# Performance work log

Measured on AMD Instinct MI355X. Metric: run time of the kernel, lower is better.

The kernel has to match this reference:

```python
import jax, jax.numpy as jnp
import numpy as np

DIM = 1024
NUM_HEADS = 16
HEAD_DIM = DIM // NUM_HEADS
SCALE = HEAD_DIM ** -0.5


def setup_inputs() -> dict:
    key = jax.random.key(0)
    ks = jax.random.split(key, 9)
    s = DIM ** -0.5
    return {
        'x_q': jax.random.normal(ks[0], (4, 2048, DIM), dtype=jnp.float32),
        'wq': jax.random.normal(ks[1], (DIM, DIM), dtype=jnp.float32) * s,
        'bq': jax.random.normal(ks[2], (DIM,), dtype=jnp.float32) * 0.02,
        'wk': jax.random.normal(ks[3], (DIM, DIM), dtype=jnp.float32) * s,
        'bk': jax.random.normal(ks[4], (DIM,), dtype=jnp.float32) * 0.02,
        'wv': jax.random.normal(ks[5], (DIM, DIM), dtype=jnp.float32) * s,
        'bv': jax.random.normal(ks[6], (DIM,), dtype=jnp.float32) * 0.02,
        'wo': jax.random.normal(ks[7], (DIM, DIM), dtype=jnp.float32) * s,
        'bo': jax.random.normal(ks[8], (DIM,), dtype=jnp.float32) * 0.02,
    }


def reference(x_q, wq, bq, wk, bk, wv, bv, wo, bo):
    B, N, C = x_q.shape
    H, c = NUM_HEADS, HEAD_DIM
    # torch nn.Linear: y = x @ W.T + b, W is [out, in]
    q = (x_q @ wq.T + bq).reshape(B, N, H, c).transpose(0, 2, 1, 3)  # [B,H,N,c]
    k = (x_q @ wk.T + bk).reshape(B, N, H, c).transpose(0, 2, 1, 3)
    v = (x_q @ wv.T + bv).reshape(B, N, H, c).transpose(0, 2, 1, 3)
    attn = jnp.einsum('bhqc,bhkc->bhqk', q, k) * SCALE  # [B,H,N,N]
    attn = jax.nn.softmax(attn, axis=-1)
    out = jnp.einsum('bhqk,bhkc->bhqc', attn, v)  # [B,H,N,c]
    out = out.transpose(0, 2, 1, 3).reshape(B, N, C)
    return out @ wo.T + bo
```

## Files before the change

### kernel.cpp

```cpp
#include <hip/hip_runtime.h>
#include <hip/hip_bf16.h>

typedef __bf16 bf16x8 __attribute__((ext_vector_type(8)));
typedef __bf16 bf16x4 __attribute__((ext_vector_type(4)));
typedef short short4v __attribute__((ext_vector_type(4)));
typedef float f32x4 __attribute__((ext_vector_type(4)));

#define QSCALE 0.18033688011112042f

__device__ __forceinline__ void gload16(const void* g, void* l) {
  __builtin_amdgcn_global_load_lds(
      (const __attribute__((address_space(1))) uint32_t*)g,
      (__attribute__((address_space(3))) uint32_t*)l, 16, 0, 0);
}

__device__ __forceinline__ unsigned bf16bits(float f) {
  union { __bf16 h; unsigned short u; } c; c.h = (__bf16)f; return c.u;
}

__device__ __forceinline__ float exp2_raw(float x) {
  float r;
  asm("v_exp_f32 %0, %1" : "=v"(r) : "v"(x));
  return r;
}

__device__ __forceinline__ f32x4 mfma16(bf16x4 a, bf16x4 b, f32x4 c) {
#if __has_builtin(__builtin_amdgcn_mfma_f32_16x16x16bf16_1k)
  union { bf16x4 h; short4v s; } ua, ub;
  ua.h = a; ub.h = b;
  return __builtin_amdgcn_mfma_f32_16x16x16bf16_1k(ua.s, ub.s, c, 0, 0, 0);
#else
  asm("v_mfma_f32_16x16x16_bf16 %0, %1, %2, %0" : "+v"(c) : "v"(a), "v"(b));
  return c;
#endif
}

__global__ __launch_bounds__(256) void cast_all(
    const float* __restrict__ x, const float* __restrict__ wq, const float* __restrict__ wk,
    const float* __restrict__ wv, const float* __restrict__ wo,
    __bf16* __restrict__ xbf, __bf16* __restrict__ wqb, __bf16* __restrict__ wkb,
    __bf16* __restrict__ wvb, __bf16* __restrict__ wob) {
  int b = blockIdx.x;
  const float* src;
  __bf16* dst;
  int i;
  if (b < 4096) {
    src = x; dst = xbf; i = b * 256 + threadIdx.x;
  } else {
    int s = (b - 4096) >> 9;
    i = ((b - 4096) & 511) * 256 + threadIdx.x;
    src = (s == 0) ? wq : (s == 1) ? wk : (s == 2) ? wv : wo;
    dst = (s == 0) ? wqb : (s == 1) ? wkb : (s == 2) ? wvb : wob;
  }
  const float4* p = (const float4*)src;
  float4 a = p[2 * i], c = p[2 * i + 1];
  bf16x8 v;
  v[0] = (__bf16)a.x; v[1] = (__bf16)a.y; v[2] = (__bf16)a.z; v[3] = (__bf16)a.w;
  v[4] = (__bf16)c.x; v[5] = (__bf16)c.y; v[6] = (__bf16)c.z; v[7] = (__bf16)c.w;
  ((bf16x8*)dst)[i] = v;
}

template <int MODE>
__global__ __launch_bounds__(256) void gemm_nt(
    const __bf16* __restrict__ A,
    const __bf16* __restrict__ W0, const __bf16* __restrict__ W1, const __bf16* __restrict__ W2,
    const float* __restrict__ b0, const float* __restrict__ b1, const float* __restrict__ b2,
    __bf16* __restrict__ o0, __bf16* __restrict__ o1, __bf16* __restrict__ o2,
    float* __restrict__ of) {
  __shared__ __bf16 lA[128 * 32];
  __shared__ __bf16 lB[128 * 32];
  const int t = threadIdx.x;
  const int lane = t & 63;
  const int w = t >> 6;
  const int wr = w >> 1, wc = w & 1;
  const int l16 = lane & 15, l4 = lane >> 4;
  const int m0 = blockIdx.x * 128;
  int sel, bn;
  if (MODE == 0) { sel = blockIdx.y >> 3; bn = (blockIdx.y & 7) * 128; }
  else           { sel = 0;               bn = blockIdx.y * 128; }
  const __bf16* W   = (sel == 0) ? W0 : (sel == 1) ? W1 : W2;
  const float* bias = (sel == 0) ? b0 : (sel == 1) ? b1 : b2;

  f32x4 acc[4][4] = {};

  for (int k0 = 0; k0 < 1024; k0 += 32) {
    __syncthreads();
#pragma unroll
    for (int i = 0; i < 2; i++) {
      int c = t + i * 256;
      int r = c >> 2, cp = c & 3;
      gload16(A + (size_t)(m0 + r) * 1024 + k0 + cp * 8, lA + c * 8);
      gload16(W + (size_t)(bn + r) * 1024 + k0 + cp * 8, lB + c * 8);
    }
    __syncthreads();
    bf16x8 af[4], bfr[4];
#pragma unroll
    for (int m = 0; m < 4; m++)
      af[m] = *(const bf16x8*)(lA + (wr * 64 + m * 16 + l16) * 32 + l4 * 8);
#pragma unroll
    for (int n = 0; n < 4; n++)
      bfr[n] = *(const bf16x8*)(lB + (wc * 64 + n * 16 + l16) * 32 + l4 * 8);
#pragma unroll
    for (int m = 0; m < 4; m++)
#pragma unroll
      for (int n = 0; n < 4; n++)
        acc[m][n] = __builtin_amdgcn_mfma_f32_16x16x32_bf16(af[m], bfr[n], acc[m][n], 0, 0, 0);
  }

  const float scl = (MODE == 0 && sel == 0) ? QSCALE : 1.0f;
  __bf16* outp = (sel == 0) ? o0 : (sel == 1) ? o1 : o2;
#pragma unroll
  for (int n = 0; n < 4; n++) {
    const int col = bn + wc * 64 + n * 16 + l16;
    const float bv = bias[col];
    if (MODE == 0 && sel == 2) {
      const int h = col >> 6, hc = col & 63;
#pragma unroll
      for (int m = 0; m < 4; m++) {
        const int nnb = m0 + wr * 64 + m * 16 + l4 * 4;
        const int b_ = nnb >> 11, nn = nnb & 2047;
        ushort4 ov;
        ov.x = (unsigned short)bf16bits(acc[m][n][0] + bv);
        ov.y = (unsigned short)bf16bits(acc[m][n][1] + bv);
        ov.z = (unsigned short)bf16bits(acc[m][n][2] + bv);
        ov.w = (unsigned short)bf16bits(acc[m][n][3] + bv);
        *(ushort4*)(outp + ((size_t)(b_ * 16 + h) * 64 + hc) * 2048 + nn) = ov;
      }
    } else {
#pragma unroll
      for (int m = 0; m < 4; m++) {
#pragma unroll
        for (int j = 0; j < 4; j++) {
          const int row = m0 + wr * 64 + m * 16 + l4 * 4 + j;
          float v = acc[m][n][j] + bv;
          if (MODE == 0) {
            v *= scl;
            int b_ = row >> 11, nn = row & 2047;
            int h = col >> 6, hc = col & 63;
            outp[(((size_t)(b_ * 16 + h)) * 2048 + nn) * 64 + hc] = (__bf16)v;
          } else {
            of[(size_t)row * 1024 + col] = v;
          }
        }
      }
    }
  }
}

__global__ __launch_bounds__(256) void attn_fwd(const __bf16* __restrict__ Q,
                                                const __bf16* __restrict__ K,
                                                const __bf16* __restrict__ Vt,
                                                __bf16* __restrict__ O) {
  __shared__ __bf16 sm[16384];
  const int flat = blockIdx.x;
  const int wg = (flat & 7) * 128 + (flat >> 3);
  const int bh = wg >> 4;
  const int q0 = (wg & 15) * 128;
  const __bf16* Qh = Q + (size_t)bh * 2048 * 64;
  const __bf16* Kh = K + (size_t)bh * 2048 * 64;
  const __bf16* Vh = Vt + (size_t)bh * 64 * 2048;
  const int t = threadIdx.x, lane = t & 63, w = t >> 6;
  const int l16 = lane & 15, l4 = lane >> 4;

  bf16x8 qf[2][2];
#pragma unroll
  for (int st = 0; st < 2; st++)
#pragma unroll
    for (int kk = 0; kk < 2; kk++)
      qf[st][kk] = *(const bf16x8*)(Qh + (size_t)(q0 + w * 32 + st * 16 + l16) * 64 + kk * 32 + l4 * 8);

  f32x4 ao[2][4] = {};
  float rs[2] = {0.f, 0.f};

  const int rdbase = l4 * 512 + l16 * 8;
  const int vbase = 8192 + (l4 >> 1) * 512 + l16 * 8 + (l4 & 1) * 4;

#pragma unroll
  for (int i = 0; i < 2; i++) {
    int ic = w * 2 + i;
    gload16(Kh + (size_t)lane * 64 + ic * 8, sm + ic * 512 + lane * 8);
    gload16(Vh + (size_t)lane * 2048 + ic * 8, sm + 8192 + ic * 512 + lane * 8);
  }
  __syncthreads();

#define ATTN_STEP(CUR, TNEXT)                                                         \
  {                                                                                   \
    const __bf16* lds = sm + (CUR) * 4096;                                            \
    if ((TNEXT) < 32) {                                                               \
      const int kvn = (TNEXT) * 64;                                                   \
      __bf16* dst = sm + ((CUR) ^ 1) * 4096;                                          \
      _Pragma("unroll")                                                               \
      for (int i = 0; i < 2; i++) {                                                   \
        int ic = w * 2 + i;                                                           \
        gload16(Kh + (size_t)(kvn + lane) * 64 + ic * 8, dst + ic * 512 + lane * 8);  \
        gload16(Vh + (size_t)lane * 2048 + kvn + ic * 8, dst + 8192 + ic * 512 + lane * 8); \
      }                                                                               \
    }                                                                                 \
    f32x4 s[2][4] = {};                                                               \
    __builtin_amdgcn_s_setprio(1);                                                    \
    _Pragma("unroll")                                                                 \
    for (int kk = 0; kk < 2; kk++) {                                                  \
      _Pragma("unroll")                                                               \
      for (int n = 0; n < 4; n++) {                                                   \
        bf16x8 kf = *(const bf16x8*)(lds + rdbase + kk * 2048 + n * 128);             \
        _Pragma("unroll")                                                             \
        for (int st = 0; st < 2; st++)                                                \
          s[st][n] = __builtin_amdgcn_mfma_f32_16x16x32_bf16(kf, qf[st][kk], s[st][n], 0, 0, 0); \
      }                                                                               \
    }                                                                                 \
    __builtin_amdgcn_s_setprio(0);                                                    \
    bf16x4 vf[4][4];                                                                  \
    _Pragma("unroll")                                                                 \
    for (int n = 0; n < 4; n++)                                                       \
      _Pragma("unroll")                                                               \
      for (int cb = 0; cb < 4; cb++)                                                  \
        vf[n][cb] = *(const bf16x4*)(lds + vbase + n * 1024 + cb * 128);              \
    __builtin_amdgcn_s_setprio(1);                                                    \
    _Pragma("unroll")                                                                 \
    for (int st = 0; st < 2; st++) {                                                  \
      _Pragma("unroll")                                                               \
      for (int n = 0; n < 4; n++) {                                                   \
        float p0 = exp2_raw(s[st][n][0]), p1 = exp2_raw(s[st][n][1]);                 \
        float p2 = exp2_raw(s[st][n][2]), p3 = exp2_raw(s[st][n][3]);                 \
        rs[st] += (p0 + p1) + (p2 + p3);                                              \
        bf16x4 pc;                                                                    \
        pc[0] = (__bf16)p0; pc[1] = (__bf16)p1;                                       \
        pc[2] = (__bf16)p2; pc[3] = (__bf16)p3;                                       \
        _Pragma("unroll")                                                             \
        for (int cb = 0; cb < 4; cb++)                                                \
          ao[st][cb] = mfma16(vf[n][cb], pc, ao[st][cb]);                             \
      }                                                                               \
    }                                                                                 \
    __builtin_amdgcn_s_setprio(0);                                                    \
    __syncthreads();                                                                  \
  }

  for (int tkv = 0; tkv < 32; tkv += 2) {
    ATTN_STEP(0, tkv + 1);
    ATTN_STEP(1, tkv + 2);
  }
#undef ATTN_STEP

  const int b_ = bh >> 4, h = bh & 15;
#pragma unroll
  for (int st = 0; st < 2; st++) {
    float ps = rs[st];
    ps += __shfl_xor(ps, 16);
    ps += __shfl_xor(ps, 32);
    const float inv = 1.f / ps;
    const int qrow = q0 + w * 32 + st * 16 + l16;
#pragma unroll
    for (int cb = 0; cb < 4; cb++) {
      ushort4 ov;
      ov.x = (unsigned short)bf16bits(ao[st][cb][0] * inv);
      ov.y = (unsigned short)bf16bits(ao[st][cb][1] * inv);
      ov.z = (unsigned short)bf16bits(ao[st][cb][2] * inv);
      ov.w = (unsigned short)bf16bits(ao[st][cb][3] * inv);
      *(ushort4*)(O + ((size_t)b_ * 2048 + qrow) * 1024 + h * 64 + cb * 16 + l4 * 4) = ov;
    }
  }
}

extern "C" void kernel_launch(void* const* d_in, const int* in_sizes, int n_in,
                              void* d_out, int out_size, void* d_ws, size_t ws_size,
                              hipStream_t stream) {
  const float* x  = (const float*)d_in[0];
  const float* wq = (const float*)d_in[1];
  const float* bq = (const float*)d_in[2];
  const float* wk = (const float*)d_in[3];
  const float* bk = (const float*)d_in[4];
  const float* wv = (const float*)d_in[5];
  const float* bv = (const float*)d_in[6];
  const float* wo = (const float*)d_in[7];
  const float* bo = (const float*)d_in[8];
  float* out = (float*)d_out;

  const size_t NX = 8388608;
  const size_t NW = 1048576;
  __bf16* xbf = (__bf16*)d_ws;
  __bf16* wqb = xbf + NX;
  __bf16* wkb = wqb + NW;
  __bf16* wvb = wkb + NW;
  __bf16* wob = wvb + NW;
  __bf16* Qb  = wob + NW;
  __bf16* Kb  = Qb + NX;
  __bf16* Vtb = Kb + NX;

  cast_all<<<6144, 256, 0, stream>>>(x, wq, wk, wv, wo, xbf, wqb, wkb, wvb, wob);

  gemm_nt<0><<<dim3(64, 24), 256, 0, stream>>>(xbf, wqb, wkb, wvb, bq, bk, bv,
                                               Qb, Kb, Vtb, nullptr);
  attn_fwd<<<1024, 256, 0, stream>>>(Qb, Kb, Vtb, xbf );
  gemm_nt<1><<<dim3(64, 8), 256, 0, stream>>>(xbf, wob, nullptr, nullptr, bo, nullptr, nullptr,
                                              nullptr, nullptr, nullptr, out);
}
```

Measured before the change: 202.1 us.

## Use 16x16x32 MFMA for PV with permlane-swapped packed P and MFMA row sums

Replaces the 16x16x16 bf16 MFMAs for the P·V product with 16x16x32 MFMAs. The probabilities are packed with v_cvt_pk_bf16 and rearranged across lanes with permlane32/16 swaps so they match the wider K layout. The softmax row sum now comes from an extra MFMA against a ones vector, replacing the VALU adds and the final cross-lane shuffles. The aim is to halve the PV MFMA instruction count and cut scalar VALU work, at the cost of extra permlane instructions and one extra MFMA per group. The row sums now come from bf16-rounded P rather than fp32 P.

```diff
diff --git a/kernel.cpp b/kernel.cpp
--- a/kernel.cpp
+++ b/kernel.cpp
@@ -2,9 +2,8 @@
 #include <hip/hip_bf16.h>
 
 typedef __bf16 bf16x8 __attribute__((ext_vector_type(8)));
-typedef __bf16 bf16x4 __attribute__((ext_vector_type(4)));
-typedef short short4v __attribute__((ext_vector_type(4)));
 typedef float f32x4 __attribute__((ext_vector_type(4)));
+typedef unsigned int u32x4 __attribute__((ext_vector_type(4)));
 
 #define QSCALE 0.18033688011112042f
 
@@ -24,16 +23,14 @@
   return r;
 }
 
-__device__ __forceinline__ f32x4 mfma16(bf16x4 a, bf16x4 b, f32x4 c) {
-#if __has_builtin(__builtin_amdgcn_mfma_f32_16x16x16bf16_1k)
-  union { bf16x4 h; short4v s; } ua, ub;
-  ua.h = a; ub.h = b;
-  return __builtin_amdgcn_mfma_f32_16x16x16bf16_1k(ua.s, ub.s, c, 0, 0, 0);
-#else
-  asm("v_mfma_f32_16x16x16_bf16 %0, %1, %2, %0" : "+v"(c) : "v"(a), "v"(b));
-  return c;
-#endif
-}
+__device__ __forceinline__ unsigned cvt_pk_bf16(float a, float b) {
+  unsigned r;
+  asm("v_cvt_pk_bf16_f32 %0, %1, %2" : "=v"(r) : "v"(a), "v"(b));
+  return r;
+}
+
+#define SWAPL32(a, b) asm("v_permlane32_swap_b32 %0, %1" : "+v"(a), "+v"(b))
+#define SWAPL16(a, b) asm("v_permlane16_swap_b32 %0, %1" : "+v"(a), "+v"(b))
 
 __global__ __launch_bounds__(256) void cast_all(
     const float* __restrict__ x, const float* __restrict__ wq, const float* __restrict__ wk,
@@ -170,10 +167,13 @@
       qf[st][kk] = *(const bf16x8*)(Qh + (size_t)(q0 + w * 32 + st * 16 + l16) * 64 + kk * 32 + l4 * 8);
 
   f32x4 ao[2][4] = {};
-  float rs[2] = {0.f, 0.f};
+  f32x4 rs4[2] = {};
+  bf16x8 onesf;
+#pragma unroll
+  for (int i = 0; i < 8; i++) onesf[i] = (__bf16)1.0f;
 
   const int rdbase = l4 * 512 + l16 * 8;
-  const int vbase = 8192 + (l4 >> 1) * 512 + l16 * 8 + (l4 & 1) * 4;
+  const int vb = 8192 + l4 * 512 + l16 * 8;
 
 #pragma unroll
   for (int i = 0; i < 2; i++) {
@@ -209,26 +209,39 @@
       }                                                                               \
     }                                                                                 \
     __builtin_amdgcn_s_setprio(0);                                                    \
-    bf16x4 vf[4][4];                                                                  \
+    bf16x8 vf[2][4];                                                                  \
     _Pragma("unroll")                                                                 \
-    for (int n = 0; n < 4; n++)                                                       \
+    for (int g = 0; g < 2; g++)                                                       \
       _Pragma("unroll")                                                               \
       for (int cb = 0; cb < 4; cb++)                                                  \
-        vf[n][cb] = *(const bf16x4*)(lds + vbase + n * 1024 + cb * 128);              \
+        vf[g][cb] = *(const bf16x8*)(lds + vb + g * 2048 + cb * 128);                 \
+    u32x4 pk[2][2];                                                                   \
+    _Pragma("unroll")                                                                 \
+    for (int st = 0; st < 2; st++) {                                                  \
+      _Pragma("unroll")                                                               \
+      for (int g = 0; g < 2; g++) {                                                   \
+        float p0 = exp2_raw(s[st][2 * g][0]),     p1 = exp2_raw(s[st][2 * g][1]);     \
+        float p2 = exp2_raw(s[st][2 * g][2]),     p3 = exp2_raw(s[st][2 * g][3]);     \
+        float p4 = exp2_raw(s[st][2 * g + 1][0]), p5 = exp2_raw(s[st][2 * g + 1][1]); \
+        float p6 = exp2_raw(s[st][2 * g + 1][2]), p7 = exp2_raw(s[st][2 * g + 1][3]); \
+        unsigned c00 = cvt_pk_bf16(p0, p1), c01 = cvt_pk_bf16(p2, p3);                \
+        unsigned c10 = cvt_pk_bf16(p4, p5), c11 = cvt_pk_bf16(p6, p7);                \
+        SWAPL32(c00, c10); SWAPL32(c01, c11);                                         \
+        SWAPL16(c00, c10); SWAPL16(c01, c11);                                         \
+        u32x4 tv = {c00, c01, c10, c11};                                              \
+        pk[st][g] = tv;                                                               \
+      }                                                                               \
+    }                                                                                 \
     __builtin_amdgcn_s_setprio(1);                                                    \
     _Pragma("unroll")                                                                 \
     for (int st = 0; st < 2; st++) {                                                  \
       _Pragma("unroll")                                                               \
-      for (int n = 0; n < 4; n++) {                                                   \
-        float p0 = exp2_raw(s[st][n][0]), p1 = exp2_raw(s[st][n][1]);                 \
-        float p2 = exp2_raw(s[st][n][2]), p3 = exp2_raw(s[st][n][3]);                 \
-        rs[st] += (p0 + p1) + (p2 + p3);                                              \
-        bf16x4 pc;                                                                    \
-        pc[0] = (__bf16)p0; pc[1] = (__bf16)p1;                                       \
-        pc[2] = (__bf16)p2; pc[3] = (__bf16)p3;                                       \
+      for (int g = 0; g < 2; g++) {                                                   \
+        union { u32x4 u; bf16x8 h; } cv; cv.u = pk[st][g];                            \
+        rs4[st] = __builtin_amdgcn_mfma_f32_16x16x32_bf16(onesf, cv.h, rs4[st], 0, 0, 0); \
         _Pragma("unroll")                                                             \
         for (int cb = 0; cb < 4; cb++)                                                \
-          ao[st][cb] = mfma16(vf[n][cb], pc, ao[st][cb]);                             \
+          ao[st][cb] = __builtin_amdgcn_mfma_f32_16x16x32_bf16(vf[g][cb], cv.h, ao[st][cb], 0, 0, 0); \
       }                                                                               \
     }                                                                                 \
     __builtin_amdgcn_s_setprio(0);                                                    \
@@ -244,10 +257,7 @@
   const int b_ = bh >> 4, h = bh & 15;
 #pragma unroll
   for (int st = 0; st < 2; st++) {
-    float ps = rs[st];
-    ps += __shfl_xor(ps, 16);
-    ps += __shfl_xor(ps, 32);
-    const float inv = 1.f / ps;
+    const float inv = 1.f / rs4[st][0];
     const int qrow = q0 + w * 32 + st * 16 + l16;
 #pragma unroll
     for (int cb = 0; cb < 4; cb++) {
```

Result: faster. 191.7 us (-5.1%).
